# Kernel tuning notes

Hardware: AMD Instinct MI355X
Metric: run time of the kernel (lower is better)

## Reference

```python
import jax, jax.numpy as jnp
import numpy as np

L, T, F, DIM = 16, 16384, 2, 3
N_MIN, N_MAX = 16.0, 512.0
N_PTS = 262144
# torch code builds np.int32 primes [1, 2654435761, 805459861]; 2654435761 wraps to -1640531535.
# Since T is a power of two, int32 wraparound multiply/xor followed by nonnegative mod T gives
# bit-identical indices to the int64 torch computation.
PIS = jnp.array([1, -1640531535, 805459861], dtype=jnp.int32)
# corner ordering from get_indices: corner k = a*4+b*2+c with a->dim0, b->dim1, c->dim2
OFFS = jnp.array([[(k >> 2) & 1, (k >> 1) & 1, k & 1] for k in range(8)], dtype=jnp.float32)  # (8,3)


def setup_inputs() -> dict:
    key = jax.random.key(0)
    k1, k2 = jax.random.split(key)
    x = jax.random.uniform(k1, (N_PTS, DIM), dtype=jnp.float32)
    # nn.init.uniform_(weight, a=-1e-4, b=1e-4) for each of L tables of shape (T, F)
    embeddings = jax.random.uniform(k2, (L, T, F), minval=-1e-4, maxval=1e-4, dtype=jnp.float32)
    return {"x": x, "embeddings": embeddings}


def reference(x, embeddings):
    # per-level growth factor b = exp((log Nmax - log Nmin)/L); N_l = Nmin * b**l
    b = jnp.exp((jnp.log(N_MAX) - jnp.log(N_MIN)) / L)
    N_l = N_MIN * b ** jnp.arange(L, dtype=jnp.float32)                      # (L,)
    un_x = x[None, :, :] * N_l[:, None, None]                                # (L,N,3)  (mu=0, sigma=1)
    lo = jnp.floor(un_x)
    hi = jnp.ceil(un_x)
    d = hi - lo                                                              # (L,N,3)
    nz = d != 0
    diff = jnp.where(nz, (un_x - lo) / jnp.where(nz, d, 1.0), 0.0)           # (L,N,3)

    mask = OFFS.astype(bool)[None, None]                                     # (1,1,8,3)
    corners = jnp.where(mask, hi[:, :, None, :], lo[:, :, None, :])          # (L,N,8,3)
    ci = corners.astype(jnp.int32)
    prod = ci * PIS                                                          # (L,N,8,3) wrapping int32 mul
    idx = jnp.mod(prod[..., 0] ^ prod[..., 1] ^ prod[..., 2], T)             # (L,N,8)

    # per-level table gather: (L,T,F)[ (L,N,8) ] -> (L,N,8,F)
    feats = jax.vmap(lambda emb, i: emb[i])(embeddings, idx)

    # trilinear weights: prod over dims of (diff if corner bit else 1-diff)
    w = jnp.prod(jnp.where(mask, diff[:, :, None, :], 1.0 - diff[:, :, None, :]), axis=-1)  # (L,N,8)
    c = jnp.einsum('lnc,lncf->lnf', w, feats)                                # (L,N,F)
    return jnp.transpose(c, (1, 0, 2)).reshape(x.shape[0], L * F)            # (N, L*F)
```

## Files before the change

### kernel.cpp

```cpp
#include <hip/hip_runtime.h>
#include <stdint.h>

constexpr int L_LEVELS = 16;
constexpr int T_SIZE   = 16384;
constexpr int N_PTS    = 262144;

typedef _Float16 h2 __attribute__((ext_vector_type(2)));
typedef _Float16 h4 __attribute__((ext_vector_type(4)));
typedef _Float16 h8 __attribute__((ext_vector_type(8)));

constexpr uint32_t P1_4 = 2654435761u * 4u;
constexpr uint32_t P2_4 = 805459861u * 4u;
constexpr uint32_t M4   = (T_SIZE - 1) * 4u;

__device__ __forceinline__ h2 lerp2(h2 a, h2 b, h2 t) {
    return a + t * (b - a);
}

__global__ __launch_bounds__(256) void cvt_emb(
    const float4* __restrict__ src, h4* __restrict__ dst)
{
    const int i = blockIdx.x * 256 + threadIdx.x;
    const float4 v = src[i];
    h4 w = { (_Float16)v.x, (_Float16)v.y, (_Float16)v.z, (_Float16)v.w };
    dst[i] = w;
}

__global__ __launch_bounds__(512, 4) void hash_encode_lds(
    const float* __restrict__ x,
    const h2* __restrict__ emb16,
    h2* __restrict__ ws)
{
    __shared__ h2 tab[T_SIZE];

    const int l     = blockIdx.x & (L_LEVELS - 1);
    const int chunk = blockIdx.x >> 4;
    const int t     = threadIdx.x;
    const int n0    = chunk * 4096 + t * 8;

    {
        const float4* __restrict__ s4 =
            reinterpret_cast<const float4*>(emb16 + (size_t)l * T_SIZE);
        float4* __restrict__ d4 = reinterpret_cast<float4*>(tab);
#pragma unroll
        for (int it = 0; it < 8; ++it)
            d4[it * 512 + t] = s4[it * 512 + t];
    }

    union { float4 q[6]; float f[24]; } xs;
    {
        const float4* __restrict__ xv =
            reinterpret_cast<const float4*>(x + (size_t)n0 * 3);
#pragma unroll
        for (int i = 0; i < 6; ++i) xs.q[i] = xv[i];
    }

    __syncthreads();

    const float Nl = 16.0f * exp2f((float)l * 0.3125f);
    const char* __restrict__ tb = reinterpret_cast<const char*>(tab);

    union { h2 r[8]; float4 q[2]; } res;

#pragma unroll
    for (int p = 0; p < 8; ++p) {
        const float u0 = xs.f[3 * p + 0] * Nl;
        const float u1 = xs.f[3 * p + 1] * Nl;
        const float u2 = xs.f[3 * p + 2] * Nl;

        const float fl0 = floorf(u0), fl1 = floorf(u1), fl2 = floorf(u2);
        const float df0 = u0 - fl0, df1 = u1 - fl1, df2 = u2 - fl2;

        const uint32_t q0 = ((uint32_t)(int32_t)fl0) << 2;
        const uint32_t q1 = ((uint32_t)(int32_t)fl1) * P1_4;
        const uint32_t q2 = ((uint32_t)(int32_t)fl2) * P2_4;
        const uint32_t d0 = (q0 ^ (q0 + 4u))   & M4;
        const uint32_t d1 = (q1 ^ (q1 + P1_4)) & M4;
        const uint32_t d2 = (q2 ^ (q2 + P2_4)) & M4;

        uint32_t off = (q0 ^ q1 ^ q2) & M4;

        constexpr int gray[8] = {0, 1, 3, 2, 6, 7, 5, 4};
        h2 f[8];
#pragma unroll
        for (int j = 0; j < 8; ++j) {
            f[gray[j]] = *reinterpret_cast<const h2*>(tb + off);
            if (j < 7) {
                const int tog = gray[j] ^ gray[j + 1];
                off ^= (tog == 4) ? d0 : (tog == 2) ? d1 : d2;
            }
        }

        const _Float16 h0 = (_Float16)df0, h1 = (_Float16)df1, hz = (_Float16)df2;
        const h2 t0 = {h0, h0}, t1 = {h1, h1}, t2 = {hz, hz};
        h2 e0 = lerp2(f[0], f[1], t2);
        h2 e1 = lerp2(f[2], f[3], t2);
        h2 e2 = lerp2(f[4], f[5], t2);
        h2 e3 = lerp2(f[6], f[7], t2);
        h2 g0 = lerp2(e0, e1, t1);
        h2 g1 = lerp2(e2, e3, t1);
        res.r[p] = lerp2(g0, g1, t0);
    }

    float4* ws4 = reinterpret_cast<float4*>(ws + (size_t)l * N_PTS + n0);
    ws4[0] = res.q[0];
    ws4[1] = res.q[1];
}

__global__ __launch_bounds__(256) void transpose_lnf_nlf(
    const h2* __restrict__ ws,
    float4* __restrict__ out4)
{
    __shared__ h2 tile[L_LEVELS][514];
    const int t    = threadIdx.x;
    const int base = blockIdx.x * 512;

#pragma unroll
    for (int l = 0; l < L_LEVELS; ++l) {
        const float2 v = *reinterpret_cast<const float2*>(
            ws + (size_t)l * N_PTS + base + 2 * t);
        *reinterpret_cast<float2*>(&tile[l][2 * t]) = v;
    }
    __syncthreads();

#pragma unroll
    for (int i = 0; i < L_LEVELS; ++i) {
        const int flat = i * 256 + t;
        const int p  = flat >> 3;
        const int lp = flat & 7;
        h2 a = tile[2 * lp][p];
        h2 b = tile[2 * lp + 1][p];
        float4 o = { (float)a.x, (float)a.y, (float)b.x, (float)b.y };
        out4[(size_t)(base + p) * 8 + lp] = o;
    }
}

__global__ __launch_bounds__(512, 4) void hash_encode_direct(
    const float* __restrict__ x,
    const float* __restrict__ emb,
    float2* __restrict__ out)
{
    __shared__ h2 tab[T_SIZE];

    const int l     = blockIdx.x & (L_LEVELS - 1);
    const int chunk = blockIdx.x >> 4;
    const int t     = threadIdx.x;
    const int n0    = chunk * 4096 + t * 8;

    {
        const float4* __restrict__ src =
            reinterpret_cast<const float4*>(emb + (size_t)l * T_SIZE * 2);
        h8* __restrict__ d8 = reinterpret_cast<h8*>(tab);
#pragma unroll
        for (int it = 0; it < 8; ++it) {
            const int i = it * 512 + t;
            float4 a = src[2 * i];
            float4 b = src[2 * i + 1];
            h8 w = { (_Float16)a.x, (_Float16)a.y, (_Float16)a.z, (_Float16)a.w,
                     (_Float16)b.x, (_Float16)b.y, (_Float16)b.z, (_Float16)b.w };
            d8[i] = w;
        }
    }
    union { float4 q[6]; float f[24]; } xs;
    {
        const float4* __restrict__ xv =
            reinterpret_cast<const float4*>(x + (size_t)n0 * 3);
#pragma unroll
        for (int i = 0; i < 6; ++i) xs.q[i] = xv[i];
    }
    __syncthreads();

    const float Nl = 16.0f * exp2f((float)l * 0.3125f);
    const char* __restrict__ tb = reinterpret_cast<const char*>(tab);

#pragma unroll
    for (int p = 0; p < 8; ++p) {
        const float u0 = xs.f[3 * p + 0] * Nl;
        const float u1 = xs.f[3 * p + 1] * Nl;
        const float u2 = xs.f[3 * p + 2] * Nl;
        const float fl0 = floorf(u0), fl1 = floorf(u1), fl2 = floorf(u2);
        const float df0 = u0 - fl0, df1 = u1 - fl1, df2 = u2 - fl2;
        const uint32_t q0 = ((uint32_t)(int32_t)fl0) << 2;
        const uint32_t q1 = ((uint32_t)(int32_t)fl1) * P1_4;
        const uint32_t q2 = ((uint32_t)(int32_t)fl2) * P2_4;
        const uint32_t d0 = (q0 ^ (q0 + 4u))   & M4;
        const uint32_t d1 = (q1 ^ (q1 + P1_4)) & M4;
        const uint32_t d2 = (q2 ^ (q2 + P2_4)) & M4;
        uint32_t off = (q0 ^ q1 ^ q2) & M4;
        constexpr int gray[8] = {0, 1, 3, 2, 6, 7, 5, 4};
        h2 f[8];
#pragma unroll
        for (int j = 0; j < 8; ++j) {
            f[gray[j]] = *reinterpret_cast<const h2*>(tb + off);
            if (j < 7) {
                const int tog = gray[j] ^ gray[j + 1];
                off ^= (tog == 4) ? d0 : (tog == 2) ? d1 : d2;
            }
        }
        const _Float16 h0 = (_Float16)df0, h1 = (_Float16)df1, hz = (_Float16)df2;
        const h2 t0 = {h0, h0}, t1 = {h1, h1}, t2 = {hz, hz};
        h2 e0 = lerp2(f[0], f[1], t2);
        h2 e1 = lerp2(f[2], f[3], t2);
        h2 e2 = lerp2(f[4], f[5], t2);
        h2 e3 = lerp2(f[6], f[7], t2);
        h2 g0 = lerp2(e0, e1, t1);
        h2 g1 = lerp2(e2, e3, t1);
        h2 r  = lerp2(g0, g1, t0);
        out[(size_t)(n0 + p) * L_LEVELS + l] =
            make_float2((float)r.x, (float)r.y);
    }
}

extern "C" void kernel_launch(void* const* d_in, const int* in_sizes, int n_in,
                              void* d_out, int out_size, void* d_ws, size_t ws_size,
                              hipStream_t stream) {
    const float* x   = (const float*)d_in[0];
    const float* emb = (const float*)d_in[1];

    const size_t ws_arr_bytes = (size_t)N_PTS * L_LEVELS * sizeof(h2);
    const size_t emb16_bytes  = (size_t)L_LEVELS * T_SIZE * sizeof(h2);

    if (ws_size >= ws_arr_bytes + emb16_bytes) {
        h2* ws    = (h2*)d_ws;
        h2* emb16 = (h2*)((char*)d_ws + ws_arr_bytes);

        cvt_emb<<<512, 256, 0, stream>>>((const float4*)emb, (h4*)emb16);
        hash_encode_lds<<<1024, 512, 0, stream>>>(x, emb16, ws);
        transpose_lnf_nlf<<<N_PTS / 512, 256, 0, stream>>>(ws, (float4*)d_out);
    } else {
        hash_encode_direct<<<1024, 512, 0, stream>>>(x, emb, (float2*)d_out);
    }
}
```

Baseline: 88.32 us.

## Fuse all levels per block and drop the transpose kernel

Each 1024-thread block now handles 1024 points across all 16 levels. It reloads the per-level fp16 table into LDS level by level, with a register prefetch of the next level's table, and writes the final (N, L*F) output directly. This removes the workspace round-trip and the separate transpose kernel. In exchange there are only 256 blocks (about one per CU), two barriers per level, and each block reloads every level table, which raises total L2 traffic for tables.

```diff
diff --git a/kernel.cpp b/kernel.cpp
--- a/kernel.cpp
+++ b/kernel.cpp
@@ -26,48 +26,46 @@
     dst[i] = w;
 }
 
-__global__ __launch_bounds__(512, 4) void hash_encode_lds(
+__global__ __launch_bounds__(1024, 4) void hash_encode_alllevels(
     const float* __restrict__ x,
     const h2* __restrict__ emb16,
-    h2* __restrict__ ws)
+    float4* __restrict__ out4)
 {
-    __shared__ h2 tab[T_SIZE];
-
-    const int l     = blockIdx.x & (L_LEVELS - 1);
-    const int chunk = blockIdx.x >> 4;
-    const int t     = threadIdx.x;
-    const int n0    = chunk * 4096 + t * 8;
-
+    __shared__ float4 tabraw[T_SIZE / 2];
+    const char* __restrict__ tb = reinterpret_cast<const char*>(tabraw);
+
+    const int t = threadIdx.x;
+    const int n = blockIdx.x * 1024 + t;
+
+    const float xv0 = x[3 * n + 0];
+    const float xv1 = x[3 * n + 1];
+    const float xv2 = x[3 * n + 2];
+
+    float4 pf[4];
     {
         const float4* __restrict__ s4 =
-            reinterpret_cast<const float4*>(emb16 + (size_t)l * T_SIZE);
-        float4* __restrict__ d4 = reinterpret_cast<float4*>(tab);
-#pragma unroll
-        for (int it = 0; it < 8; ++it)
-            d4[it * 512 + t] = s4[it * 512 + t];
-    }
-
-    union { float4 q[6]; float f[24]; } xs;
-    {
-        const float4* __restrict__ xv =
-            reinterpret_cast<const float4*>(x + (size_t)n0 * 3);
-#pragma unroll
-        for (int i = 0; i < 6; ++i) xs.q[i] = xv[i];
-    }
-
+            reinterpret_cast<const float4*>(emb16);
+#pragma unroll
+        for (int j = 0; j < 4; ++j) pf[j] = s4[j * 1024 + t];
+#pragma unroll
+        for (int j = 0; j < 4; ++j) tabraw[j * 1024 + t] = pf[j];
+    }
     __syncthreads();
 
-    const float Nl = 16.0f * exp2f((float)l * 0.3125f);
-    const char* __restrict__ tb = reinterpret_cast<const char*>(tab);
-
-    union { h2 r[8]; float4 q[2]; } res;
-
-#pragma unroll
-    for (int p = 0; p < 8; ++p) {
-        const float u0 = xs.f[3 * p + 0] * Nl;
-        const float u1 = xs.f[3 * p + 1] * Nl;
-        const float u2 = xs.f[3 * p + 2] * Nl;
-
+    h2 res[L_LEVELS];
+
+#pragma unroll
+    for (int l = 0; l < L_LEVELS; ++l) {
+        if (l < L_LEVELS - 1) {
+            const float4* __restrict__ s4 = reinterpret_cast<const float4*>(
+                emb16 + (size_t)(l + 1) * T_SIZE);
+#pragma unroll
+            for (int j = 0; j < 4; ++j) pf[j] = s4[j * 1024 + t];
+        }
+
+        const float Nl = 16.0f * exp2f((float)l * 0.3125f);
+
+        const float u0 = xv0 * Nl, u1 = xv1 * Nl, u2 = xv2 * Nl;
         const float fl0 = floorf(u0), fl1 = floorf(u1), fl2 = floorf(u2);
         const float df0 = u0 - fl0, df1 = u1 - fl1, df2 = u2 - fl2;
 
@@ -99,39 +97,21 @@
         h2 e3 = lerp2(f[6], f[7], t2);
         h2 g0 = lerp2(e0, e1, t1);
         h2 g1 = lerp2(e2, e3, t1);
-        res.r[p] = lerp2(g0, g1, t0);
-    }
-
-    float4* ws4 = reinterpret_cast<float4*>(ws + (size_t)l * N_PTS + n0);
-    ws4[0] = res.q[0];
-    ws4[1] = res.q[1];
-}
-
-__global__ __launch_bounds__(256) void transpose_lnf_nlf(
-    const h2* __restrict__ ws,
-    float4* __restrict__ out4)
-{
-    __shared__ h2 tile[L_LEVELS][514];
-    const int t    = threadIdx.x;
-    const int base = blockIdx.x * 512;
-
-#pragma unroll
-    for (int l = 0; l < L_LEVELS; ++l) {
-        const float2 v = *reinterpret_cast<const float2*>(
-            ws + (size_t)l * N_PTS + base + 2 * t);
-        *reinterpret_cast<float2*>(&tile[l][2 * t]) = v;
-    }
-    __syncthreads();
-
-#pragma unroll
-    for (int i = 0; i < L_LEVELS; ++i) {
-        const int flat = i * 256 + t;
-        const int p  = flat >> 3;
-        const int lp = flat & 7;
-        h2 a = tile[2 * lp][p];
-        h2 b = tile[2 * lp + 1][p];
-        float4 o = { (float)a.x, (float)a.y, (float)b.x, (float)b.y };
-        out4[(size_t)(base + p) * 8 + lp] = o;
+        res[l] = lerp2(g0, g1, t0);
+
+        __syncthreads();
+        if (l < L_LEVELS - 1) {
+#pragma unroll
+            for (int j = 0; j < 4; ++j) tabraw[j * 1024 + t] = pf[j];
+            __syncthreads();
+        }
+    }
+
+    float4* __restrict__ dst = out4 + (size_t)n * 8;
+#pragma unroll
+    for (int k = 0; k < 8; ++k) {
+        const h2 a = res[2 * k], b = res[2 * k + 1];
+        dst[k] = make_float4((float)a.x, (float)a.y, (float)b.x, (float)b.y);
     }
 }
 
@@ -217,16 +197,13 @@
     const float* x   = (const float*)d_in[0];
     const float* emb = (const float*)d_in[1];
 
-    const size_t ws_arr_bytes = (size_t)N_PTS * L_LEVELS * sizeof(h2);
-    const size_t emb16_bytes  = (size_t)L_LEVELS * T_SIZE * sizeof(h2);
-
-    if (ws_size >= ws_arr_bytes + emb16_bytes) {
-        h2* ws    = (h2*)d_ws;
-        h2* emb16 = (h2*)((char*)d_ws + ws_arr_bytes);
-
+    const size_t emb16_bytes = (size_t)L_LEVELS * T_SIZE * sizeof(h2);
+
+    if (ws_size >= emb16_bytes) {
+        h2* emb16 = (h2*)d_ws;
         cvt_emb<<<512, 256, 0, stream>>>((const float4*)emb, (h4*)emb16);
-        hash_encode_lds<<<1024, 512, 0, stream>>>(x, emb16, ws);
-        transpose_lnf_nlf<<<N_PTS / 512, 256, 0, stream>>>(ws, (float4*)d_out);
+        hash_encode_alllevels<<<256, 1024, 0, stream>>>(x, emb16,
+                                                        (float4*)d_out);
     } else {
         hash_encode_direct<<<1024, 512, 0, stream>>>(x, emb, (float2*)d_out);
     }
```

Result: slower. 153.5 us (+73.8%).
